# Kernel optimization log

Hardware: AMD Instinct MI355X
Metric: run time of the kernel (lower is better)

The kernel has to match this reference:

```python
import jax, jax.numpy as jnp
import numpy as np

E = 65536          # number of edges (cell pairs)
D = 256            # hidden_dim
P = 8              # n_lr_pairs


def setup_inputs() -> dict:
    key = jax.random.key(0)
    k1, k2, k3, k4, k5, k6, k7 = jax.random.split(key, 7)
    scale = 1.0 / np.sqrt(D)
    z_src = jax.random.normal(k1, (E, D), dtype=jnp.float32)
    z_dst = jax.random.normal(k2, (E, D), dtype=jnp.float32)
    lr_pair_idx = jax.random.randint(k3, (E,), 0, P, dtype=jnp.int64)
    # Per-LR-pair Linear(D, D): y = x @ W.T + b  (torch convention, W: [out, in])
    W_lr = jax.random.normal(k4, (P, D, D), dtype=jnp.float32) * scale
    b_lr = jax.random.normal(k5, (P, D), dtype=jnp.float32) * scale
    # nn.Bilinear(D, D, 1): weight [1, D, D], bias [1]
    W_bil = jax.random.normal(k6, (1, D, D), dtype=jnp.float32) * scale
    b_bil = jax.random.normal(k7, (1,), dtype=jnp.float32) * scale
    return {"z_src": z_src, "z_dst": z_dst, "W_lr": W_lr, "b_lr": b_lr,
            "W_bil": W_bil, "b_bil": b_bil, "lr_pair_idx": lr_pair_idx}


def _forward(z_src, z_dst, W_lr, b_lr, W_bil, b_bil, lr_pair_idx):
    # Per-LR-pair linear projection of z_src (MoE-style routing).
    # Fixed small loop over P experts; each iteration is a dense GEMM over
    # all E edges, masked to the edges routed to that pair. All idx values
    # lie in [0, P), so the zeros-init in the original is fully overwritten.
    z_proj = jnp.zeros_like(z_src)
    for p in range(P):
        mask = (lr_pair_idx == p)[:, None]                      # [E, 1]
        y_p = z_src @ W_lr[p].T + b_lr[p]                       # [E, D]
        z_proj = jnp.where(mask, y_p, z_proj)
    # Bilinear scoring: score_e = z_proj_e @ W_bil[0] @ z_dst_e + b_bil
    t = z_proj @ W_bil[0]                                       # [E, D]
    scores = jnp.sum(t * z_dst, axis=-1, keepdims=True) + b_bil  # [E, 1]
    return scores


def reference(z_src, z_dst, W_lr, b_lr, W_bil, b_bil, lr_pair_idx):
    return _forward(z_src, z_dst, W_lr, b_lr, W_bil, b_bil, lr_pair_idx)
```

## Files before the change

kernel.cpp:

```cpp
#include <hip/hip_runtime.h>
#include <hip/hip_bf16.h>
#include <cstddef>

#define NE 65536
#define ND 256
#define NP 8
#define RBLK 64
#define EPB (NE / RBLK)
#define TR 32
#define MAXT 2056

typedef short bf16x8 __attribute__((ext_vector_type(8)));
typedef float f32x4  __attribute__((ext_vector_type(4)));
typedef const __attribute__((address_space(1))) unsigned int* gas_t;
typedef __attribute__((address_space(3))) unsigned int* las_t;

__device__ __forceinline__ unsigned short f2bf(float f) {
  unsigned int u = __float_as_uint(f);
  u += 0x7FFFu + ((u >> 16) & 1u);
  return (unsigned short)(u >> 16);
}

__device__ __forceinline__ int sniff_is32(const void* idxraw, int* lflag) {
  int tid = threadIdx.x;
  if (tid == 0) *lflag = 0;
  __syncthreads();
  const unsigned int* w = (const unsigned int*)idxraw;
  unsigned int val = w[((blockIdx.x & 63) * 256 + (tid & 255)) * 2 + 1];
  if (__any(val != 0) && (tid & 63) == 0) atomicOr(lflag, 1);
  __syncthreads();
  return *lflag;
}
__device__ __forceinline__ int load_idx(const void* idxraw, int is32, int e) {
  return is32 ? ((const int*)idxraw)[e] : (int)((const long long*)idxraw)[e];
}

__global__ __launch_bounds__(256) void k_hist(const void* __restrict__ idxraw,
                                              int* __restrict__ counts) {
  __shared__ int h[NP];
  __shared__ int lflag;
  int tid = threadIdx.x;
  int is32 = sniff_is32(idxraw, &lflag);
  if (tid < NP) h[tid] = 0;
  __syncthreads();
  int base = blockIdx.x * EPB;
#pragma unroll
  for (int i = 0; i < EPB / 256; ++i) {
    int p = load_idx(idxraw, is32, base + tid + i * 256);
    atomicAdd(&h[p], 1);
  }
  __syncthreads();
  if (tid < NP) counts[blockIdx.x * NP + tid] = h[tid];
}

__global__ __launch_bounds__(64) void k_scan(const int* __restrict__ counts,
                                             int* __restrict__ hdr,
                                             int* __restrict__ bases) {
  __shared__ int cnt[NP];
  __shared__ int off[NP + 1];
  int q = threadIdx.x;
  if (q < NP) {
    int s = 0;
    for (int b = 0; b < RBLK; ++b) s += counts[b * NP + q];
    cnt[q] = s;
  }
  __syncthreads();
  if (q == 0) {
    int o = 0, tt = 0;
    for (int p = 0; p < NP; ++p) {
      off[p] = o; hdr[p] = o; hdr[9 + p] = tt;
      o += cnt[p];
      tt += (cnt[p] + TR - 1) / TR;
    }
    off[NP] = o; hdr[NP] = o; hdr[9 + NP] = tt;
  }
  __syncthreads();
  if (q < NP) {
    int run = off[q];
    for (int b = 0; b < RBLK; ++b) {
      bases[b * NP + q] = run;
      run += counts[b * NP + q];
    }
  }
}

__global__ __launch_bounds__(256) void k_scatter(const void* __restrict__ idxraw,
                                                 const int* __restrict__ bases,
                                                 int* __restrict__ perm) {
  __shared__ int cur[NP];
  __shared__ int lflag;
  int tid = threadIdx.x;
  int is32 = sniff_is32(idxraw, &lflag);
  if (tid < NP) cur[tid] = bases[blockIdx.x * NP + tid];
  __syncthreads();
  int base = blockIdx.x * EPB;
#pragma unroll
  for (int i = 0; i < EPB / 256; ++i) {
    int e = base + tid + i * 256;
    int p = load_idx(idxraw, is32, e);
    int slot = atomicAdd(&cur[p], 1);
    perm[slot] = e;
  }
}

__global__ __launch_bounds__(256) void k_prep(const float* __restrict__ Wbil,
                                              const float* __restrict__ blr,
                                              unsigned short* __restrict__ WbT,
                                              float* __restrict__ v) {
  int b = blockIdx.x, t = threadIdx.x;
  if (b < 32) {
    int s = b * 256 + t;
    int kt = s >> 10, c = (s >> 6) & 15, l = s & 63;
    int col = c * 16 + (l & 15);
    int k0 = kt * 32 + (l >> 4) * 8;
    union { uint4 u; unsigned short h[8]; } uu;
#pragma unroll
    for (int j = 0; j < 8; ++j)
      uu.h[j] = f2bf(Wbil[(k0 + j) * ND + col]);
    *(uint4*)(WbT + (size_t)s * 8) = uu.u;
  } else {
    int p = b - 32;
    float s = 0.f;
    for (int k = 0; k < ND; ++k)
      s = fmaf(blr[p * ND + k], Wbil[k * ND + t], s);
    v[p * ND + t] = s;
  }
}

__global__ __launch_bounds__(256) void k_cpre(const float* __restrict__ Wlr,
                                              const unsigned short* __restrict__ WbT,
                                              unsigned short* __restrict__ Cst) {
  __shared__ unsigned short aF[2048 * 8];
  int blk = blockIdx.x;
  int p = blk >> 2;
  int i0 = (blk & 3) * 64;
  int tid = threadIdx.x;
  const float* Wp = Wlr + (size_t)p * ND * ND;
#pragma unroll
  for (int it = 0; it < 8; ++it) {
    int s = tid + it * 256;
    int kt = s >> 8, r = (s >> 6) & 3, l = s & 63;
    int i = r * 16 + (l & 15);
    int k0 = kt * 32 + (l >> 4) * 8;
    union { uint4 u; unsigned short h[8]; } uu;
#pragma unroll
    for (int j = 0; j < 8; ++j)
      uu.h[j] = f2bf(Wp[(size_t)(k0 + j) * ND + i0 + i]);
    *(uint4*)(aF + (size_t)s * 8) = uu.u;
  }
  __syncthreads();
  int w = tid >> 6, l = tid & 63;
  f32x4 zero = {0.f, 0.f, 0.f, 0.f};
  f32x4 acc[16];
#pragma unroll
  for (int c = 0; c < 16; ++c) acc[c] = zero;
  for (int kt = 0; kt < 8; ++kt) {
    bf16x8 a = *(const bf16x8*)(aF + (size_t)((kt * 4 + w) * 64 + l) * 8);
#pragma unroll
    for (int c = 0; c < 16; ++c) {
      bf16x8 bb = *(const bf16x8*)(WbT + (size_t)((kt * 16 + c) * 64 + l) * 8);
      acc[c] = __builtin_amdgcn_mfma_f32_16x16x32_bf16(a, bb, acc[c], 0, 0, 0);
    }
  }
  unsigned short* Cp = Cst + (size_t)p * ND * ND;
#pragma unroll
  for (int c = 0; c < 16; ++c) {
#pragma unroll
    for (int q = 0; q < 4; ++q) {
      int i = i0 + w * 16 + ((l >> 4) * 4) + q;
      int j = c * 16 + (l & 15);
      int pos = ((i >> 5) * 16 + (j >> 4)) * 512 + (((i >> 3) & 3) * 16 + (j & 15)) * 8 + (i & 7);
      Cp[pos] = f2bf(acc[c][q]);
    }
  }
}

__global__ __launch_bounds__(512, 4) void k_main(const float* __restrict__ zsrc,
                                                 const float* __restrict__ zdst,
                                                 const int* __restrict__ perm,
                                                 const int* __restrict__ hdr,
                                                 const unsigned short* __restrict__ Cst,
                                                 const float* __restrict__ v,
                                                 const float* __restrict__ bbil,
                                                 float* __restrict__ out) {
  __shared__ float zsF[TR * 256];
  __shared__ float zdF[TR * 256];
  __shared__ float red[8][TR];
  __shared__ int eids[TR];
  __shared__ int shdr[18];
  int tid = threadIdx.x;
  if (tid < 18) shdr[tid] = hdr[tid];
  __syncthreads();
  int bid = blockIdx.x;
  if (bid >= shdr[9 + NP]) return;
  int p = 0;
  while (p < NP - 1 && bid >= shdr[9 + p + 1]) ++p;
  int t = bid - shdr[9 + p];
  int cnt = shdr[p + 1] - shdr[p];
  int ebase = shdr[p] + t * TR;
  int nrow = cnt - t * TR; if (nrow > TR) nrow = TR;
  if (tid < TR) eids[tid] = perm[ebase + (tid < nrow ? tid : nrow - 1)];
  __syncthreads();
  int w = tid >> 6, l = tid & 63;

#pragma unroll
  for (int i = 0; i < 4; ++i) {
    int row = w * 4 + i;
    int e = eids[row];
    int s = row & 3;
    unsigned srcoff = ((((unsigned)(l >> 1) ^ (unsigned)s) << 5) | ((unsigned)(l & 1) << 4));
    const float* gs = zsrc + (size_t)e * ND + (srcoff >> 2);
    const float* gd = zdst + (size_t)e * ND + (srcoff >> 2);
    __builtin_amdgcn_global_load_lds((gas_t)(const void*)gs,
                                     (las_t)(void*)((char*)zsF + row * 1024), 16, 0, 0);
    __builtin_amdgcn_global_load_lds((gas_t)(const void*)gd,
                                     (las_t)(void*)((char*)zdF + row * 1024), 16, 0, 0);
  }
  __syncthreads();

  const unsigned short* Cp = Cst + (size_t)p * ND * ND;
  f32x4 zero = {0.f, 0.f, 0.f, 0.f};
  f32x4 acc[2][2];
#pragma unroll
  for (int sr = 0; sr < 2; ++sr)
#pragma unroll
    for (int cl = 0; cl < 2; ++cl) acc[sr][cl] = zero;
  int hh = l >> 4, rr = l & 15;
#pragma unroll
  for (int kt = 0; kt < 8; ++kt) {
    bf16x8 a[2];
#pragma unroll
    for (int sr = 0; sr < 2; ++sr) {
      int row = sr * 16 + rr;
      unsigned pidx = (unsigned)((kt * 4 + hh) ^ (row & 3));
      const char* bp = (const char*)zsF + row * 1024 + (pidx << 5);
      float4 f0 = *(const float4*)(bp);
      float4 f1 = *(const float4*)(bp + 16);
      union { bf16x8 vv; unsigned short h[8]; } ua;
      ua.h[0] = f2bf(f0.x); ua.h[1] = f2bf(f0.y); ua.h[2] = f2bf(f0.z); ua.h[3] = f2bf(f0.w);
      ua.h[4] = f2bf(f1.x); ua.h[5] = f2bf(f1.y); ua.h[6] = f2bf(f1.z); ua.h[7] = f2bf(f1.w);
      a[sr] = ua.vv;
    }
#pragma unroll
    for (int cl = 0; cl < 2; ++cl) {
      bf16x8 bb = *(const bf16x8*)(Cp + (size_t)((kt * 16 + (w * 2 + cl)) * 64 + l) * 8);
#pragma unroll
      for (int sr = 0; sr < 2; ++sr)
        acc[sr][cl] = __builtin_amdgcn_mfma_f32_16x16x32_bf16(a[sr], bb, acc[sr][cl], 0, 0, 0);
    }
  }

  float vloc[2];
#pragma unroll
  for (int cl = 0; cl < 2; ++cl)
    vloc[cl] = v[p * ND + (w * 2 + cl) * 16 + rr];
#pragma unroll
  for (int sr = 0; sr < 2; ++sr) {
#pragma unroll
    for (int q = 0; q < 4; ++q) {
      int row = sr * 16 + hh * 4 + q;
      int s = row & 3;
      float sv = 0.f;
#pragma unroll
      for (int cl = 0; cl < 2; ++cl) {
        int col = (w * 2 + cl) * 16 + rr;
        unsigned byte = (unsigned)(row * 1024) + ((((unsigned)(col >> 3) ^ (unsigned)s) << 5) | ((unsigned)(col & 7) << 2));
        float zv = *(const float*)((const char*)zdF + byte);
        sv = fmaf(acc[sr][cl][q] + vloc[cl], zv, sv);
      }
      sv += __shfl_xor(sv, 1, 64);
      sv += __shfl_xor(sv, 2, 64);
      sv += __shfl_xor(sv, 4, 64);
      sv += __shfl_xor(sv, 8, 64);
      if (rr == 0) red[w][row] = sv;
    }
  }
  __syncthreads();
  if (tid < TR && tid < nrow) {
    float sc = bbil[0];
#pragma unroll
    for (int ww = 0; ww < 8; ++ww) sc += red[ww][tid];
    out[eids[tid]] = sc;
  }
}

extern "C" void kernel_launch(void* const* d_in, const int* in_sizes, int n_in,
                              void* d_out, int out_size, void* d_ws, size_t ws_size,
                              hipStream_t stream) {
  const float* zsrc = (const float*)d_in[0];
  const float* zdst = (const float*)d_in[1];
  const float* Wlr  = (const float*)d_in[2];
  const float* blr  = (const float*)d_in[3];
  const float* Wbil = (const float*)d_in[4];
  const float* bbil = (const float*)d_in[5];
  const void*  idx  = (const void*)d_in[6];
  float* out = (float*)d_out;

  char* ws = (char*)d_ws;
  int* hdr    = (int*)ws;
  int* counts = (int*)(ws + 4096);
  int* bases  = (int*)(ws + 8192);
  int* perm   = (int*)(ws + 16384);
  unsigned short* WbT = (unsigned short*)(ws + 16384 + (size_t)NE * 4);
  float* v = (float*)(ws + 16384 + (size_t)NE * 4 + 131072);
  unsigned short* Cst = (unsigned short*)(ws + 16384 + (size_t)NE * 4 + 131072 + 8192);

  k_prep<<<40, 256, 0, stream>>>(Wbil, blr, WbT, v);
  k_hist<<<RBLK, 256, 0, stream>>>(idx, counts);
  k_scan<<<1, 64, 0, stream>>>(counts, hdr, bases);
  k_scatter<<<RBLK, 256, 0, stream>>>(idx, bases, perm);
  k_cpre<<<32, 256, 0, stream>>>(Wlr, WbT, Cst);
  k_main<<<MAXT, 512, 0, stream>>>(zsrc, zdst, perm, hdr, Cst, v, bbil, out);
}
```

Baseline: 92.21 us.

## Make k_main persistent with double-buffered async tile loads and register-cached weights

The main kernel becomes persistent: 256 blocks each walk a contiguous chunk of tiles instead of one block per tile. The gather of z_src/z_dst rows for the next tile goes into a second LDS buffer, overlapped with the MFMA work on the current tile through explicit vmcnt waits. The per-expert weight fragments and bias vector stay in registers and are reloaded only when the expert changes, and the LDS swizzle is reworked to 16-byte granularity. The cost is fewer resident blocks per CU, larger register and LDS use, and possible load imbalance with only 256 blocks.

```diff
diff --git a/kernel.cpp b/kernel.cpp
--- a/kernel.cpp
+++ b/kernel.cpp
@@ -8,7 +8,8 @@
 #define RBLK 64
 #define EPB (NE / RBLK)
 #define TR 32
-#define MAXT 2056
+#define NBLK 256
+#define MAXCH 9
 
 typedef short bf16x8 __attribute__((ext_vector_type(8)));
 typedef float f32x4  __attribute__((ext_vector_type(4)));
@@ -175,7 +176,7 @@
   }
 }
 
-__global__ __launch_bounds__(512, 4) void k_main(const float* __restrict__ zsrc,
+__global__ __launch_bounds__(512, 2) void k_main(const float* __restrict__ zsrc,
                                                  const float* __restrict__ zdst,
                                                  const int* __restrict__ perm,
                                                  const int* __restrict__ hdr,
@@ -183,105 +184,153 @@
                                                  const float* __restrict__ v,
                                                  const float* __restrict__ bbil,
                                                  float* __restrict__ out) {
-  __shared__ float zsF[TR * 256];
-  __shared__ float zdF[TR * 256];
+  __shared__ float zbuf[2][16384];
   __shared__ float red[8][TR];
-  __shared__ int eids[TR];
+  __shared__ int eidsAll[MAXCH * TR];
+  __shared__ int pExp[MAXCH], pNrow[MAXCH];
   __shared__ int shdr[18];
   int tid = threadIdx.x;
   if (tid < 18) shdr[tid] = hdr[tid];
   __syncthreads();
-  int bid = blockIdx.x;
-  if (bid >= shdr[9 + NP]) return;
-  int p = 0;
-  while (p < NP - 1 && bid >= shdr[9 + p + 1]) ++p;
-  int t = bid - shdr[9 + p];
-  int cnt = shdr[p + 1] - shdr[p];
-  int ebase = shdr[p] + t * TR;
-  int nrow = cnt - t * TR; if (nrow > TR) nrow = TR;
-  if (tid < TR) eids[tid] = perm[ebase + (tid < nrow ? tid : nrow - 1)];
-  __syncthreads();
+  int ntiles = shdr[17];
+  int chunk = (ntiles + NBLK - 1) / NBLK;
+  int t0 = blockIdx.x * chunk;
+  if (t0 >= ntiles) return;
+  int t1 = t0 + chunk; if (t1 > ntiles) t1 = ntiles;
+  for (int j = tid; j < (t1 - t0) * TR; j += 512) {
+    int tl = j >> 5, tt = t0 + tl;
+    int p = 0;
+    while (p < NP - 1 && tt >= shdr[9 + p + 1]) ++p;
+    int ebase = shdr[p] + (tt - shdr[9 + p]) * TR;
+    int cend = shdr[p + 1];
+    int r = j & 31;
+    int re = ebase + r; if (re > cend - 1) re = cend - 1;
+    eidsAll[j] = perm[re];
+    if (r == 0) {
+      pExp[tl] = p;
+      int nr = cend - ebase; pNrow[tl] = nr > TR ? TR : nr;
+    }
+  }
+  __syncthreads();
+
   int w = tid >> 6, l = tid & 63;
-
-#pragma unroll
-  for (int i = 0; i < 4; ++i) {
-    int row = w * 4 + i;
-    int e = eids[row];
-    int s = row & 3;
-    unsigned srcoff = ((((unsigned)(l >> 1) ^ (unsigned)s) << 5) | ((unsigned)(l & 1) << 4));
-    const float* gs = zsrc + (size_t)e * ND + (srcoff >> 2);
-    const float* gd = zdst + (size_t)e * ND + (srcoff >> 2);
-    __builtin_amdgcn_global_load_lds((gas_t)(const void*)gs,
-                                     (las_t)(void*)((char*)zsF + row * 1024), 16, 0, 0);
-    __builtin_amdgcn_global_load_lds((gas_t)(const void*)gd,
-                                     (las_t)(void*)((char*)zdF + row * 1024), 16, 0, 0);
-  }
-  __syncthreads();
-
-  const unsigned short* Cp = Cst + (size_t)p * ND * ND;
+  int hh = l >> 4, rr = l & 15;
+  float bb0 = bbil[0];
+
+#define STAGE(TT, BSEL)                                                          \
+  {                                                                              \
+    int _tl = (TT) - t0;                                                         \
+    char* _zb = (char*)&zbuf[(BSEL)][0];                                         \
+    _Pragma("unroll")                                                            \
+    for (int _i = 0; _i < 4; ++_i) {                                             \
+      int _row = w * 4 + _i;                                                     \
+      int _e = eidsAll[_tl * TR + _row];                                         \
+      unsigned _s = (unsigned)(_row & 7);                                        \
+      unsigned _sf = (((unsigned)l ^ _s) << 2);                                  \
+      const float* _gs = zsrc + (size_t)_e * ND + _sf;                           \
+      const float* _gd = zdst + (size_t)_e * ND + _sf;                           \
+      __builtin_amdgcn_global_load_lds((gas_t)(const void*)_gs,                  \
+          (las_t)(void*)(_zb + _row * 1024), 16, 0, 0);                          \
+      __builtin_amdgcn_global_load_lds((gas_t)(const void*)_gd,                  \
+          (las_t)(void*)(_zb + 32768 + _row * 1024), 16, 0, 0);                  \
+    }                                                                            \
+  }
+
+  STAGE(t0, 0);
+  int bsel = 0;
+  int curP = -1;
+  bf16x8 bfr[2][8];
+  float vloc[2];
   f32x4 zero = {0.f, 0.f, 0.f, 0.f};
-  f32x4 acc[2][2];
-#pragma unroll
-  for (int sr = 0; sr < 2; ++sr)
-#pragma unroll
-    for (int cl = 0; cl < 2; ++cl) acc[sr][cl] = zero;
-  int hh = l >> 4, rr = l & 15;
-#pragma unroll
-  for (int kt = 0; kt < 8; ++kt) {
-    bf16x8 a[2];
+
+  for (int tt = t0; tt < t1; ++tt) {
+    int tl = tt - t0;
+    if (tt + 1 < t1) {
+      STAGE(tt + 1, bsel ^ 1);
+      asm volatile("s_waitcnt vmcnt(8)" ::: "memory");
+    } else {
+      asm volatile("s_waitcnt vmcnt(0)" ::: "memory");
+    }
+    __builtin_amdgcn_sched_barrier(0);
+    __builtin_amdgcn_s_barrier();
+
+    int p = pExp[tl];
+    if (p != curP) {
+      curP = p;
+      const unsigned short* Cp = Cst + (size_t)p * ND * ND;
+#pragma unroll
+      for (int cl = 0; cl < 2; ++cl) {
+#pragma unroll
+        for (int kt = 0; kt < 8; ++kt)
+          bfr[cl][kt] = *(const bf16x8*)(Cp + (size_t)((kt * 16 + (w * 2 + cl)) * 64 + l) * 8);
+        vloc[cl] = v[p * ND + (w * 2 + cl) * 16 + rr];
+      }
+    }
+
+    const char* zs = (const char*)&zbuf[bsel][0];
+    const char* zd = (const char*)&zbuf[bsel][8192];
+    f32x4 acc[2][2];
+#pragma unroll
+    for (int sr = 0; sr < 2; ++sr)
+#pragma unroll
+      for (int cl = 0; cl < 2; ++cl) acc[sr][cl] = zero;
+
+#pragma unroll
+    for (int kt = 0; kt < 8; ++kt) {
+      bf16x8 a[2];
+#pragma unroll
+      for (int sr = 0; sr < 2; ++sr) {
+        int row = sr * 16 + rr;
+        unsigned s = (unsigned)(row & 7);
+        unsigned G0 = (unsigned)((kt * 4 + hh) * 2);
+        float4 f0 = *(const float4*)(zs + row * 1024 + ((G0 ^ s) << 4));
+        float4 f1 = *(const float4*)(zs + row * 1024 + (((G0 + 1) ^ s) << 4));
+        union { bf16x8 vv; unsigned short h[8]; } ua;
+        ua.h[0] = f2bf(f0.x); ua.h[1] = f2bf(f0.y); ua.h[2] = f2bf(f0.z); ua.h[3] = f2bf(f0.w);
+        ua.h[4] = f2bf(f1.x); ua.h[5] = f2bf(f1.y); ua.h[6] = f2bf(f1.z); ua.h[7] = f2bf(f1.w);
+        a[sr] = ua.vv;
+      }
+#pragma unroll
+      for (int cl = 0; cl < 2; ++cl)
+#pragma unroll
+        for (int sr = 0; sr < 2; ++sr)
+          acc[sr][cl] = __builtin_amdgcn_mfma_f32_16x16x32_bf16(a[sr], bfr[cl][kt], acc[sr][cl], 0, 0, 0);
+    }
+
 #pragma unroll
     for (int sr = 0; sr < 2; ++sr) {
-      int row = sr * 16 + rr;
-      unsigned pidx = (unsigned)((kt * 4 + hh) ^ (row & 3));
-      const char* bp = (const char*)zsF + row * 1024 + (pidx << 5);
-      float4 f0 = *(const float4*)(bp);
-      float4 f1 = *(const float4*)(bp + 16);
-      union { bf16x8 vv; unsigned short h[8]; } ua;
-      ua.h[0] = f2bf(f0.x); ua.h[1] = f2bf(f0.y); ua.h[2] = f2bf(f0.z); ua.h[3] = f2bf(f0.w);
-      ua.h[4] = f2bf(f1.x); ua.h[5] = f2bf(f1.y); ua.h[6] = f2bf(f1.z); ua.h[7] = f2bf(f1.w);
-      a[sr] = ua.vv;
-    }
-#pragma unroll
-    for (int cl = 0; cl < 2; ++cl) {
-      bf16x8 bb = *(const bf16x8*)(Cp + (size_t)((kt * 16 + (w * 2 + cl)) * 64 + l) * 8);
-#pragma unroll
-      for (int sr = 0; sr < 2; ++sr)
-        acc[sr][cl] = __builtin_amdgcn_mfma_f32_16x16x32_bf16(a[sr], bb, acc[sr][cl], 0, 0, 0);
-    }
-  }
-
-  float vloc[2];
-#pragma unroll
-  for (int cl = 0; cl < 2; ++cl)
-    vloc[cl] = v[p * ND + (w * 2 + cl) * 16 + rr];
-#pragma unroll
-  for (int sr = 0; sr < 2; ++sr) {
-#pragma unroll
-    for (int q = 0; q < 4; ++q) {
-      int row = sr * 16 + hh * 4 + q;
-      int s = row & 3;
-      float sv = 0.f;
-#pragma unroll
-      for (int cl = 0; cl < 2; ++cl) {
-        int col = (w * 2 + cl) * 16 + rr;
-        unsigned byte = (unsigned)(row * 1024) + ((((unsigned)(col >> 3) ^ (unsigned)s) << 5) | ((unsigned)(col & 7) << 2));
-        float zv = *(const float*)((const char*)zdF + byte);
-        sv = fmaf(acc[sr][cl][q] + vloc[cl], zv, sv);
+#pragma unroll
+      for (int q = 0; q < 4; ++q) {
+        int row = sr * 16 + hh * 4 + q;
+        unsigned s = (unsigned)(row & 7);
+        float sv = 0.f;
+#pragma unroll
+        for (int cl = 0; cl < 2; ++cl) {
+          int col = (w * 2 + cl) * 16 + rr;
+          unsigned byte = (unsigned)(row * 1024) +
+                          ((((unsigned)(col >> 2) ^ s) << 4) | ((unsigned)(col & 3) << 2));
+          float zv = *(const float*)(zd + byte);
+          sv = fmaf(acc[sr][cl][q] + vloc[cl], zv, sv);
+        }
+        sv += __shfl_xor(sv, 1, 64);
+        sv += __shfl_xor(sv, 2, 64);
+        sv += __shfl_xor(sv, 4, 64);
+        sv += __shfl_xor(sv, 8, 64);
+        if (rr == 0) red[w][row] = sv;
       }
-      sv += __shfl_xor(sv, 1, 64);
-      sv += __shfl_xor(sv, 2, 64);
-      sv += __shfl_xor(sv, 4, 64);
-      sv += __shfl_xor(sv, 8, 64);
-      if (rr == 0) red[w][row] = sv;
-    }
-  }
-  __syncthreads();
-  if (tid < TR && tid < nrow) {
-    float sc = bbil[0];
-#pragma unroll
-    for (int ww = 0; ww < 8; ++ww) sc += red[ww][tid];
-    out[eids[tid]] = sc;
-  }
+    }
+    asm volatile("s_waitcnt lgkmcnt(0)" ::: "memory");
+    __builtin_amdgcn_sched_barrier(0);
+    __builtin_amdgcn_s_barrier();
+    if (tid < TR && tid < pNrow[tl]) {
+      float sc = bb0;
+#pragma unroll
+      for (int ww = 0; ww < 8; ++ww) sc += red[ww][tid];
+      out[eidsAll[tl * TR + tid]] = sc;
+    }
+    bsel ^= 1;
+  }
+#undef STAGE
 }
 
 extern "C" void kernel_launch(void* const* d_in, const int* in_sizes, int n_in,
@@ -310,5 +359,5 @@
   k_scan<<<1, 64, 0, stream>>>(counts, hdr, bases);
   k_scatter<<<RBLK, 256, 0, stream>>>(idx, bases, perm);
   k_cpre<<<32, 256, 0, stream>>>(Wlr, WbT, Cst);
-  k_main<<<MAXT, 512, 0, stream>>>(zsrc, zdst, perm, hdr, Cst, v, bbil, out);
-}
+  k_main<<<NBLK, 512, 0, stream>>>(zsrc, zdst, perm, hdr, Cst, v, bbil, out);
+}
```

Result: no change. 93.43 us (+1.3%).

## Merge prep kernels and store gathered rows as bf16 in LDS

Applied to the files above, without the earlier changes.

Merges k_prep with k_hist, and k_scatter with k_cpre, into two launches that branch on block index, removing two kernel launches and their serialization gaps. In k_main, the gathered z_src/z_dst rows are loaded into registers, converted to bf16 and written into swizzled LDS layouts, replacing the direct global-to-LDS fp32 copies. This halves LDS per block, which allows raising the launch bound to 8 blocks per CU. Both operands are now rounded to bf16 (z_dst previously stayed fp32), and the loads are no longer asynchronous DMA into LDS.

```diff
diff --git a/kernel.cpp b/kernel.cpp
--- a/kernel.cpp
+++ b/kernel.cpp
@@ -12,45 +12,68 @@
 
 typedef short bf16x8 __attribute__((ext_vector_type(8)));
 typedef float f32x4  __attribute__((ext_vector_type(4)));
-typedef const __attribute__((address_space(1))) unsigned int* gas_t;
-typedef __attribute__((address_space(3))) unsigned int* las_t;
 
 __device__ __forceinline__ unsigned short f2bf(float f) {
   unsigned int u = __float_as_uint(f);
   u += 0x7FFFu + ((u >> 16) & 1u);
   return (unsigned short)(u >> 16);
 }
-
-__device__ __forceinline__ int sniff_is32(const void* idxraw, int* lflag) {
+__device__ __forceinline__ float bf2f(unsigned short h) {
+  return __uint_as_float(((unsigned int)h) << 16);
+}
+__device__ __forceinline__ int load_idx(const void* idxraw, int is32, int e) {
+  return is32 ? ((const int*)idxraw)[e] : (int)((const long long*)idxraw)[e];
+}
+__device__ __forceinline__ int sniff_is32(const void* idxraw, int* lflag, int bsel) {
   int tid = threadIdx.x;
   if (tid == 0) *lflag = 0;
   __syncthreads();
   const unsigned int* w = (const unsigned int*)idxraw;
-  unsigned int val = w[((blockIdx.x & 63) * 256 + (tid & 255)) * 2 + 1];
+  unsigned int val = w[((bsel & 63) * 256 + tid) * 2 + 1];
   if (__any(val != 0) && (tid & 63) == 0) atomicOr(lflag, 1);
   __syncthreads();
   return *lflag;
 }
-__device__ __forceinline__ int load_idx(const void* idxraw, int is32, int e) {
-  return is32 ? ((const int*)idxraw)[e] : (int)((const long long*)idxraw)[e];
-}
-
-__global__ __launch_bounds__(256) void k_hist(const void* __restrict__ idxraw,
+
+__global__ __launch_bounds__(256) void k_pre0(const float* __restrict__ Wbil,
+                                              const float* __restrict__ blr,
+                                              const void* __restrict__ idxraw,
+                                              unsigned short* __restrict__ WbT,
+                                              float* __restrict__ v,
                                               int* __restrict__ counts) {
-  __shared__ int h[NP];
-  __shared__ int lflag;
-  int tid = threadIdx.x;
-  int is32 = sniff_is32(idxraw, &lflag);
-  if (tid < NP) h[tid] = 0;
-  __syncthreads();
-  int base = blockIdx.x * EPB;
-#pragma unroll
-  for (int i = 0; i < EPB / 256; ++i) {
-    int p = load_idx(idxraw, is32, base + tid + i * 256);
-    atomicAdd(&h[p], 1);
-  }
-  __syncthreads();
-  if (tid < NP) counts[blockIdx.x * NP + tid] = h[tid];
+  int b = blockIdx.x, t = threadIdx.x;
+  if (b < 32) {
+    int s = b * 256 + t;
+    int kt = s >> 10, c = (s >> 6) & 15, l = s & 63;
+    int col = c * 16 + (l & 15);
+    int k0 = kt * 32 + (l >> 4) * 8;
+    union { uint4 u; unsigned short h[8]; } uu;
+#pragma unroll
+    for (int j = 0; j < 8; ++j)
+      uu.h[j] = f2bf(Wbil[(k0 + j) * ND + col]);
+    *(uint4*)(WbT + (size_t)s * 8) = uu.u;
+  } else if (b < 40) {
+    int p = b - 32;
+    float s = 0.f;
+    for (int k = 0; k < ND; ++k)
+      s = fmaf(blr[p * ND + k], Wbil[k * ND + t], s);
+    v[p * ND + t] = s;
+  } else {
+    __shared__ int h[NP];
+    __shared__ int lflag;
+    int hb = b - 40;
+    int is32 = sniff_is32(idxraw, &lflag, hb);
+    if (t < NP) h[t] = 0;
+    __syncthreads();
+    int base = hb * EPB;
+#pragma unroll
+    for (int i = 0; i < EPB / 256; ++i) {
+      int p = load_idx(idxraw, is32, base + t + i * 256);
+      atomicAdd(&h[p], 1);
+    }
+    __syncthreads();
+    if (t < NP) counts[hb * NP + t] = h[t];
+  }
 }
 
 __global__ __launch_bounds__(64) void k_scan(const int* __restrict__ counts,
@@ -84,57 +107,33 @@
   }
 }
 
-__global__ __launch_bounds__(256) void k_scatter(const void* __restrict__ idxraw,
-                                                 const int* __restrict__ bases,
-                                                 int* __restrict__ perm) {
-  __shared__ int cur[NP];
-  __shared__ int lflag;
-  int tid = threadIdx.x;
-  int is32 = sniff_is32(idxraw, &lflag);
-  if (tid < NP) cur[tid] = bases[blockIdx.x * NP + tid];
-  __syncthreads();
-  int base = blockIdx.x * EPB;
-#pragma unroll
-  for (int i = 0; i < EPB / 256; ++i) {
-    int e = base + tid + i * 256;
-    int p = load_idx(idxraw, is32, e);
-    int slot = atomicAdd(&cur[p], 1);
-    perm[slot] = e;
-  }
-}
-
-__global__ __launch_bounds__(256) void k_prep(const float* __restrict__ Wbil,
-                                              const float* __restrict__ blr,
-                                              unsigned short* __restrict__ WbT,
-                                              float* __restrict__ v) {
-  int b = blockIdx.x, t = threadIdx.x;
-  if (b < 32) {
-    int s = b * 256 + t;
-    int kt = s >> 10, c = (s >> 6) & 15, l = s & 63;
-    int col = c * 16 + (l & 15);
-    int k0 = kt * 32 + (l >> 4) * 8;
-    union { uint4 u; unsigned short h[8]; } uu;
-#pragma unroll
-    for (int j = 0; j < 8; ++j)
-      uu.h[j] = f2bf(Wbil[(k0 + j) * ND + col]);
-    *(uint4*)(WbT + (size_t)s * 8) = uu.u;
-  } else {
-    int p = b - 32;
-    float s = 0.f;
-    for (int k = 0; k < ND; ++k)
-      s = fmaf(blr[p * ND + k], Wbil[k * ND + t], s);
-    v[p * ND + t] = s;
-  }
-}
-
-__global__ __launch_bounds__(256) void k_cpre(const float* __restrict__ Wlr,
-                                              const unsigned short* __restrict__ WbT,
-                                              unsigned short* __restrict__ Cst) {
+__global__ __launch_bounds__(256) void k_sc2(const void* __restrict__ idxraw,
+                                             const int* __restrict__ bases,
+                                             int* __restrict__ perm,
+                                             const float* __restrict__ Wlr,
+                                             const unsigned short* __restrict__ WbT,
+                                             unsigned short* __restrict__ Cst) {
   __shared__ unsigned short aF[2048 * 8];
-  int blk = blockIdx.x;
+  int b = blockIdx.x, tid = threadIdx.x;
+  if (b < 64) {
+    __shared__ int cur[NP];
+    __shared__ int lflag;
+    int is32 = sniff_is32(idxraw, &lflag, b);
+    if (tid < NP) cur[tid] = bases[b * NP + tid];
+    __syncthreads();
+    int base = b * EPB;
+#pragma unroll
+    for (int i = 0; i < EPB / 256; ++i) {
+      int e = base + tid + i * 256;
+      int p = load_idx(idxraw, is32, e);
+      int slot = atomicAdd(&cur[p], 1);
+      perm[slot] = e;
+    }
+    return;
+  }
+  int blk = b - 64;
   int p = blk >> 2;
   int i0 = (blk & 3) * 64;
-  int tid = threadIdx.x;
   const float* Wp = Wlr + (size_t)p * ND * ND;
 #pragma unroll
   for (int it = 0; it < 8; ++it) {
@@ -175,7 +174,7 @@
   }
 }
 
-__global__ __launch_bounds__(512, 4) void k_main(const float* __restrict__ zsrc,
+__global__ __launch_bounds__(512, 8) void k_main(const float* __restrict__ zsrc,
                                                  const float* __restrict__ zdst,
                                                  const int* __restrict__ perm,
                                                  const int* __restrict__ hdr,
@@ -183,8 +182,8 @@
                                                  const float* __restrict__ v,
                                                  const float* __restrict__ bbil,
                                                  float* __restrict__ out) {
-  __shared__ float zsF[TR * 256];
-  __shared__ float zdF[TR * 256];
+  __shared__ unsigned short zs[8192];
+  __shared__ unsigned short zd[8192];
   __shared__ float red[8][TR];
   __shared__ int eids[TR];
   __shared__ int shdr[18];
@@ -202,19 +201,22 @@
   if (tid < TR) eids[tid] = perm[ebase + (tid < nrow ? tid : nrow - 1)];
   __syncthreads();
   int w = tid >> 6, l = tid & 63;
-
+  int hh = l >> 4, rr = l & 15;
+
+  int kt0 = l >> 3, q0 = (l >> 1) & 3, par0 = l & 1;
 #pragma unroll
   for (int i = 0; i < 4; ++i) {
     int row = w * 4 + i;
     int e = eids[row];
-    int s = row & 3;
-    unsigned srcoff = ((((unsigned)(l >> 1) ^ (unsigned)s) << 5) | ((unsigned)(l & 1) << 4));
-    const float* gs = zsrc + (size_t)e * ND + (srcoff >> 2);
-    const float* gd = zdst + (size_t)e * ND + (srcoff >> 2);
-    __builtin_amdgcn_global_load_lds((gas_t)(const void*)gs,
-                                     (las_t)(void*)((char*)zsF + row * 1024), 16, 0, 0);
-    __builtin_amdgcn_global_load_lds((gas_t)(const void*)gd,
-                                     (las_t)(void*)((char*)zdF + row * 1024), 16, 0, 0);
+    float4 fs = *(const float4*)(zsrc + (size_t)e * ND + l * 4);
+    float4 fd = *(const float4*)(zdst + (size_t)e * ND + l * 4);
+    union { unsigned long long u; unsigned short h[4]; } us, ud;
+    us.h[0] = f2bf(fs.x); us.h[1] = f2bf(fs.y); us.h[2] = f2bf(fs.z); us.h[3] = f2bf(fs.w);
+    ud.h[0] = f2bf(fd.x); ud.h[1] = f2bf(fd.y); ud.h[2] = f2bf(fd.z); ud.h[3] = f2bf(fd.w);
+    unsigned g = (unsigned)((kt0 * 2 + (row >> 4)) * 64 + (row & 15) + 16 * q0);
+    g ^= ((g >> 6) & 7u) << 1;
+    *(unsigned long long*)((char*)zs + g * 16 + par0 * 8) = us.u;
+    *(unsigned long long*)((char*)zd + ((unsigned)(row * 512 + l * 8) ^ (((unsigned)row & 7u) << 5))) = ud.u;
   }
   __syncthreads();
 
@@ -225,21 +227,14 @@
   for (int sr = 0; sr < 2; ++sr)
 #pragma unroll
     for (int cl = 0; cl < 2; ++cl) acc[sr][cl] = zero;
-  int hh = l >> 4, rr = l & 15;
 #pragma unroll
   for (int kt = 0; kt < 8; ++kt) {
     bf16x8 a[2];
 #pragma unroll
     for (int sr = 0; sr < 2; ++sr) {
-      int row = sr * 16 + rr;
-      unsigned pidx = (unsigned)((kt * 4 + hh) ^ (row & 3));
-      const char* bp = (const char*)zsF + row * 1024 + (pidx << 5);
-      float4 f0 = *(const float4*)(bp);
-      float4 f1 = *(const float4*)(bp + 16);
-      union { bf16x8 vv; unsigned short h[8]; } ua;
-      ua.h[0] = f2bf(f0.x); ua.h[1] = f2bf(f0.y); ua.h[2] = f2bf(f0.z); ua.h[3] = f2bf(f0.w);
-      ua.h[4] = f2bf(f1.x); ua.h[5] = f2bf(f1.y); ua.h[6] = f2bf(f1.z); ua.h[7] = f2bf(f1.w);
-      a[sr] = ua.vv;
+      unsigned g = (unsigned)((kt * 2 + sr) * 64 + l);
+      g ^= ((g >> 6) & 7u) << 1;
+      a[sr] = *(const bf16x8*)((const char*)zs + g * 16);
     }
 #pragma unroll
     for (int cl = 0; cl < 2; ++cl) {
@@ -259,14 +254,13 @@
 #pragma unroll
     for (int q = 0; q < 4; ++q) {
       int row = sr * 16 + hh * 4 + q;
-      int s = row & 3;
+      unsigned swz = ((unsigned)row & 7u) << 5;
       float sv = 0.f;
 #pragma unroll
       for (int cl = 0; cl < 2; ++cl) {
         int col = (w * 2 + cl) * 16 + rr;
-        unsigned byte = (unsigned)(row * 1024) + ((((unsigned)(col >> 3) ^ (unsigned)s) << 5) | ((unsigned)(col & 7) << 2));
-        float zv = *(const float*)((const char*)zdF + byte);
-        sv = fmaf(acc[sr][cl][q] + vloc[cl], zv, sv);
+        unsigned byte = ((unsigned)(row * 512 + col * 2)) ^ swz;
+        sv = fmaf(acc[sr][cl][q] + vloc[cl], bf2f(*(const unsigned short*)((const char*)zd + byte)), sv);
       }
       sv += __shfl_xor(sv, 1, 64);
       sv += __shfl_xor(sv, 2, 64);
@@ -305,10 +299,8 @@
   float* v = (float*)(ws + 16384 + (size_t)NE * 4 + 131072);
   unsigned short* Cst = (unsigned short*)(ws + 16384 + (size_t)NE * 4 + 131072 + 8192);
 
-  k_prep<<<40, 256, 0, stream>>>(Wbil, blr, WbT, v);
-  k_hist<<<RBLK, 256, 0, stream>>>(idx, counts);
+  k_pre0<<<104, 256, 0, stream>>>(Wbil, blr, idx, WbT, v, counts);
   k_scan<<<1, 64, 0, stream>>>(counts, hdr, bases);
-  k_scatter<<<RBLK, 256, 0, stream>>>(idx, bases, perm);
-  k_cpre<<<32, 256, 0, stream>>>(Wlr, WbT, Cst);
+  k_sc2<<<96, 256, 0, stream>>>(idx, bases, perm, Wlr, WbT, Cst);
   k_main<<<MAXT, 512, 0, stream>>>(zsrc, zdst, perm, hdr, Cst, v, bbil, out);
 }
```

Result: faster. 77.90 us (-15.5%).
